# Optimization experiments

Hardware: AMD Instinct MI355X
Metric: run time of the kernel (lower is better)

Reference implementation:

```python
import jax, jax.numpy as jnp
import numpy as np

OUT_F, IN_F = 8192, 4096
TOKENS = 512


def _unpack_int2_to_ternary(packed, alpha, dtype):
    # packed: [out_f, in_f//4] ints 0..255; 4 two-bit codes per byte.
    # code 0 -> -1, code 2 -> +1, codes 1/3 -> 0; then scale by per-row alpha.
    shifts = jnp.arange(4, dtype=packed.dtype) * 2  # [0,2,4,6]
    two_bit = (packed[:, :, None] >> shifts[None, None, :]) & 3  # [out_f, in_f//4, 4]
    two_bit = two_bit.reshape(packed.shape[0], -1)  # [out_f, in_f]
    sign = jnp.where(two_bit == 2, 1.0, jnp.where(two_bit == 0, -1.0, 0.0)).astype(dtype)
    return sign * alpha.astype(dtype)[:, None]


def setup_inputs() -> dict:
    key = jax.random.key(0)
    k1, k2, k3, k4 = jax.random.split(key, 4)
    x = jax.random.normal(k1, (TOKENS, IN_F), dtype=jnp.float32)
    weight_int2 = jax.random.randint(k2, (OUT_F, IN_F // 4), 0, 256, dtype=jnp.int32)
    alpha = jax.random.uniform(k3, (OUT_F,), dtype=jnp.float32, minval=0.01, maxval=0.05)
    bias = jax.random.normal(k4, (OUT_F,), dtype=jnp.float32) * 0.01
    return {"x": x, "weight_int2": weight_int2, "alpha": alpha, "bias": bias}


def reference(x, weight_int2, alpha, bias):
    W = _unpack_int2_to_ternary(weight_int2, alpha, x.dtype)  # [out_f, in_f]
    out = x @ W.T  # [tokens, out_f]
    return out + bias
```

## Files before the change

### kernel.cpp

```cpp
#include <hip/hip_runtime.h>
#include <hip/hip_bf16.h>

typedef unsigned int u32;
typedef unsigned short u16;

#define TOKENS 512
#define OUT_F  8192
#define IN_F   4096
#define KPACK  (IN_F / 4)
#define TMB 128
#define TNB 64
#define BKW 128
#define NWIN (IN_F / BKW)

typedef __attribute__((ext_vector_type(8))) short bf16x8;
typedef __attribute__((ext_vector_type(4))) float f32x4;
typedef __attribute__((ext_vector_type(16))) float f32x16;

__device__ __forceinline__ u32 pack_bf16x2(float a, float b) {
    __hip_bfloat162 h = __float22bfloat162_rn(make_float2(a, b));
    union { __hip_bfloat162 h2; u32 u; } cvt;
    cvt.h2 = h;
    return cvt.u;
}

__device__ __forceinline__ u32 decode_pair(u32 d) {
    u32 s = (__umul24(d, 0x808202u) & 0x06060606u) + 0x01000100u;
    return __builtin_amdgcn_perm(0x00003F80u, 0x0000BF80u, s);
}
__device__ __forceinline__ bf16x8 decode_frag(u32 w, int sh) {
    union { bf16x8 v; u32 u[4]; } c;
    c.u[0] = decode_pair((w >> (sh + 0)) & 0xFu);
    c.u[1] = decode_pair((w >> (sh + 4)) & 0xFu);
    c.u[2] = decode_pair((w >> (sh + 8)) & 0xFu);
    c.u[3] = decode_pair((w >> (sh + 12)) & 0xFu);
    return c.v;
}

__device__ __forceinline__ void async_ld16(const void* g, void* l) {
    __builtin_amdgcn_global_load_lds(
        (const __attribute__((address_space(1))) u32*)g,
        (__attribute__((address_space(3))) u32*)l, 16, 0, 0);
}

__global__ __launch_bounds__(256) void convert_x(const float* __restrict__ X,
                                                 u16* __restrict__ Xb) {
    int i = (blockIdx.x * 256 + threadIdx.x) * 8;
    float4 a = *(const float4*)(X + i);
    float4 b = *(const float4*)(X + i + 4);
    uint4 q;
    q.x = pack_bf16x2(a.x, a.y);
    q.y = pack_bf16x2(a.z, a.w);
    q.z = pack_bf16x2(b.x, b.y);
    q.w = pack_bf16x2(b.z, b.w);
    *(uint4*)(Xb + i) = q;
}

__global__ __launch_bounds__(256) void repack_w9(const u32* __restrict__ W2,
                                                 u32* __restrict__ W9) {
    __shared__ u32 dense[128 * 32];
    const int ngrp = blockIdx.x;
    const int kc   = blockIdx.y;
    const int t = threadIdx.x;
#pragma unroll
    for (int i = 0; i < 16; ++i) {
        int id = t + 256 * i;
        int col = id >> 5, jq = id & 31;
        uint4 wv = *(const uint4*)(W2 + (size_t)(ngrp * 128 + col) * KPACK + kc * 128 + jq * 4);
        dense[col * 32 + (jq ^ (col & 31))] =
            (wv.x & 0xFFu) | ((wv.y & 0xFFu) << 8) | ((wv.z & 0xFFu) << 16) | ((wv.w & 0xFFu) << 24);
    }
    __syncthreads();
    const u16* sp = (const u16*)dense;
#pragma unroll
    for (int p = 0; p < 4; ++p) {
        int e = t + 256 * p;
        int lane = e & 63;
        int kq = (e >> 6) & 3;
        int wp2 = (e >> 8) & 1;
        int nho = (e >> 9) & 1;
        int h = lane >> 5;
        int c0 = nho * 64 + (lane & 31), c1 = c0 + 32;
        int nb = ngrp * 2 + nho;
#pragma unroll
        for (int ws = 0; ws < 2; ++ws) {
            int wloc = wp2 * 2 + ws;
            int w = kc * 4 + wloc;
            int j0 = wloc * 8 + kq * 2;
            u32 x0 = sp[((c0 * 32 + (j0 ^ (c0 & 31))) << 1) | h];
            u32 x1 = sp[((c0 * 32 + ((j0 + 1) ^ (c0 & 31))) << 1) | h];
            u32 y0 = sp[((c1 * 32 + (j0 ^ (c1 & 31))) << 1) | h];
            u32 y1 = sp[((c1 * 32 + ((j0 + 1) ^ (c1 & 31))) << 1) | h];
            W9[((((size_t)nb * 4 + kq) * 2 + 0) * NWIN + w) * 64 + lane] = x0 | (x1 << 16);
            W9[((((size_t)nb * 4 + kq) * 2 + 1) * NWIN + w) * 64 + lane] = y0 | (y1 << 16);
        }
    }
}

__global__ __launch_bounds__(512, 4) void ternary_gemm10(
    const u16* __restrict__ Xb,
    const u32* __restrict__ W9,
    const float* __restrict__ alpha,
    const float* __restrict__ bias,
    float* __restrict__ Out)
{
    __shared__ u16 As[2][TMB * BKW];

    const int tid  = threadIdx.x;
    const int lane = tid & 63;
    const int wave = tid >> 6;
    const int kq = wave & 3;
    const int nh = wave >> 2;

    const int m0 = blockIdx.x * TMB;
    const int nb = blockIdx.y;
    const int n0 = nb * TNB;

    f32x16 acc[4];
#pragma unroll
    for (int mt = 0; mt < 4; ++mt)
#pragma unroll
        for (int i = 0; i < 16; ++i)
            acc[mt][i] = 0.f;

    const u16* gbase = Xb + (size_t)(m0 + wave * 16) * IN_F;
    u32 aoff[4];
    u32 lbase[4];
#pragma unroll
    for (int i = 0; i < 4; ++i) {
        int rr = i * 4 + (lane >> 4);
        int cd = (lane & 15) ^ (rr & 15);
        aoff[i] = rr * IN_F + cd * 8;
        lbase[i] = (wave * 16 + i * 4) * BKW;
    }

    u32 ofsA0[2];
#pragma unroll
    for (int ks = 0; ks < 2; ++ks) {
        int row = lane & 31;
        int chunk = kq * 4 + ks * 2 + (lane >> 5);
        ofsA0[ks] = row * BKW + (chunk ^ (row & 15)) * 8;
    }

    const u32* wq = W9 + ((((size_t)nb * 4 + kq) * 2 + nh) * NWIN) * 64 + lane;

    u32 wcur = wq[0];
    u32 wnext = wq[64];
#pragma unroll
    for (int i = 0; i < 4; ++i) async_ld16(gbase + aoff[i], &As[0][lbase[i]]);
    __syncthreads();

    for (int w = 0; w < NWIN; ++w) {
        const int buf = w & 1;
        if (w + 1 < NWIN) {
            const int koff = (w + 1) * BKW;
#pragma unroll
            for (int i = 0; i < 4; ++i)
                async_ld16(gbase + aoff[i] + koff, &As[buf ^ 1][lbase[i]]);
        }
        u32 wnn = 0;
        if (w + 2 < NWIN) wnn = wq[(size_t)(w + 2) * 64];

        const u16* ab = As[buf];
#pragma unroll
        for (int ks = 0; ks < 2; ++ks) {
            const u16* ap = ab + ofsA0[ks];
            bf16x8 a0 = *(const bf16x8*)(ap);
            bf16x8 a1 = *(const bf16x8*)(ap + 4096);
            bf16x8 a2 = *(const bf16x8*)(ap + 8192);
            bf16x8 a3 = *(const bf16x8*)(ap + 12288);
            bf16x8 b0 = decode_frag(wcur, ks * 16);
            acc[0] = __builtin_amdgcn_mfma_f32_32x32x16_bf16(a0, b0, acc[0], 0, 0, 0);
            acc[1] = __builtin_amdgcn_mfma_f32_32x32x16_bf16(a1, b0, acc[1], 0, 0, 0);
            acc[2] = __builtin_amdgcn_mfma_f32_32x32x16_bf16(a2, b0, acc[2], 0, 0, 0);
            acc[3] = __builtin_amdgcn_mfma_f32_32x32x16_bf16(a3, b0, acc[3], 0, 0, 0);
        }
        wcur = wnext;
        wnext = wnn;
        __syncthreads();
    }

    f32x4* red = (f32x4*)As;
#pragma unroll 1
    for (int q = 1; q < 4; ++q) {
        if (kq == q) {
            f32x4* dst = red + nh * 1024 + lane;
#pragma unroll
            for (int mt = 0; mt < 4; ++mt)
#pragma unroll
                for (int sub = 0; sub < 4; ++sub) {
                    f32x4 v = {acc[mt][sub * 4 + 0], acc[mt][sub * 4 + 1],
                               acc[mt][sub * 4 + 2], acc[mt][sub * 4 + 3]};
                    dst[(mt * 4 + sub) * 64] = v;
                }
        }
        __syncthreads();
        if (kq == 0) {
            const f32x4* src = red + nh * 1024 + lane;
#pragma unroll
            for (int mt = 0; mt < 4; ++mt)
#pragma unroll
                for (int sub = 0; sub < 4; ++sub) {
                    f32x4 v = src[(mt * 4 + sub) * 64];
#pragma unroll
                    for (int i = 0; i < 4; ++i)
                        acc[mt][sub * 4 + i] += v[i];
                }
        }
        __syncthreads();
    }

    if (kq == 0) {
        int ncol = n0 + nh * 32 + (lane & 31);
        float av = alpha[ncol];
        float bv = bias[ncol];
#pragma unroll
        for (int mt = 0; mt < 4; ++mt) {
#pragma unroll
            for (int r = 0; r < 16; ++r) {
                int row = m0 + mt * 32 + (r & 3) + 8 * (r >> 2) + 4 * (lane >> 5);
                Out[(size_t)row * OUT_F + ncol] = acc[mt][r] * av + bv;
            }
        }
    }
}

__global__ void ternary_naive(const float* __restrict__ X, const u32* __restrict__ W2,
                              const float* __restrict__ alpha, const float* __restrict__ bias,
                              float* __restrict__ Out) {
    int o  = blockIdx.x * 64 + (threadIdx.x & 63);
    int tk = blockIdx.y * 4 + (threadIdx.x >> 6);
    const float* x = X + (size_t)tk * IN_F;
    const u32* w = W2 + (size_t)o * KPACK;
    float s = 0.f;
    for (int d = 0; d < KPACK; ++d) {
        u32 b = w[d] & 0xFFu;
        const float* xp = x + d * 4;
#pragma unroll
        for (int j = 0; j < 4; ++j) {
            u32 c = (b >> (2 * j)) & 3u;
            float wv = (c == 2u) ? 1.f : ((c == 0u) ? -1.f : 0.f);
            s += xp[j] * wv;
        }
    }
    Out[(size_t)tk * OUT_F + o] = s * alpha[o] + bias[o];
}

extern "C" void kernel_launch(void* const* d_in, const int* in_sizes, int n_in,
                              void* d_out, int out_size, void* d_ws, size_t ws_size,
                              hipStream_t stream) {
    const float* x = (const float*)d_in[0];
    const u32* w2 = (const u32*)d_in[1];
    const float* alpha = (const float*)d_in[2];
    const float* bias  = (const float*)d_in[3];
    float* out = (float*)d_out;

    const size_t xb_bytes = (size_t)TOKENS * IN_F * sizeof(u16);
    const size_t w9_bytes = (size_t)OUT_F * IN_F / 4;

    if (ws_size >= xb_bytes + w9_bytes) {
        u16* xb = (u16*)d_ws;
        u32* w9 = (u32*)((char*)d_ws + xb_bytes);
        convert_x<<<(TOKENS * IN_F) / (256 * 8), 256, 0, stream>>>(x, xb);
        repack_w9<<<dim3(64, 8), 256, 0, stream>>>(w2, w9);
        ternary_gemm10<<<dim3(TOKENS / TMB, OUT_F / TNB), 512, 0, stream>>>(xb, w9, alpha, bias, out);
    } else {
        ternary_naive<<<dim3(OUT_F / 64, TOKENS / 4), 256, 0, stream>>>(x, w2, alpha, bias, out);
    }
}
```

Measured before the change: 131.3 us.

## Pipeline GEMM loads with explicit vmcnt waits and merge prep kernels

Rewrites the GEMM main loop so each window waits only for the loads it needs (s_waitcnt vmcnt(1) plus raw s_barrier) instead of a full __syncthreads drain. The next A tile's async LDS loads and the B word loads stay in flight across compute. The loop is unrolled by two with a peeled tail, and B words are loaded through inline asm. It also fuses the x-to-bf16 conversion and weight repack into one launch, saving a kernel launch. The risk is fragile hand-managed wait counts and scheduling barriers.

```diff
diff --git a/kernel.cpp b/kernel.cpp
--- a/kernel.cpp
+++ b/kernel.cpp
@@ -43,25 +43,39 @@
         (__attribute__((address_space(3))) u32*)l, 16, 0, 0);
 }
 
-__global__ __launch_bounds__(256) void convert_x(const float* __restrict__ X,
-                                                 u16* __restrict__ Xb) {
-    int i = (blockIdx.x * 256 + threadIdx.x) * 8;
-    float4 a = *(const float4*)(X + i);
-    float4 b = *(const float4*)(X + i + 4);
-    uint4 q;
-    q.x = pack_bf16x2(a.x, a.y);
-    q.y = pack_bf16x2(a.z, a.w);
-    q.z = pack_bf16x2(b.x, b.y);
-    q.w = pack_bf16x2(b.z, b.w);
-    *(uint4*)(Xb + i) = q;
-}
-
-__global__ __launch_bounds__(256) void repack_w9(const u32* __restrict__ W2,
-                                                 u32* __restrict__ W9) {
+__device__ __forceinline__ void async_b(const u32* g, u32& dst) {
+    asm volatile("global_load_dword %0, %1, off"
+                 : "=v"(dst) : "v"(g) : "memory");
+}
+
+#define VMW(N) asm volatile("s_waitcnt vmcnt(" #N ")" ::: "memory")
+
+__global__ __launch_bounds__(256) void prep(const float* __restrict__ X,
+                                            u16* __restrict__ Xb,
+                                            const u32* __restrict__ W2,
+                                            u32* __restrict__ W9) {
     __shared__ u32 dense[128 * 32];
+    const int t = threadIdx.x;
+
+    if (blockIdx.y == 8) {
+        int base = blockIdx.x * 32768 + t * 8;
+#pragma unroll
+        for (int r = 0; r < 16; ++r) {
+            int i = base + r * 2048;
+            float4 a = *(const float4*)(X + i);
+            float4 b = *(const float4*)(X + i + 4);
+            uint4 q;
+            q.x = pack_bf16x2(a.x, a.y);
+            q.y = pack_bf16x2(a.z, a.w);
+            q.z = pack_bf16x2(b.x, b.y);
+            q.w = pack_bf16x2(b.z, b.w);
+            *(uint4*)(Xb + i) = q;
+        }
+        return;
+    }
+
     const int ngrp = blockIdx.x;
     const int kc   = blockIdx.y;
-    const int t = threadIdx.x;
 #pragma unroll
     for (int i = 0; i < 16; ++i) {
         int id = t + 256 * i;
@@ -97,7 +111,7 @@
     }
 }
 
-__global__ __launch_bounds__(512, 4) void ternary_gemm10(
+__global__ __launch_bounds__(512, 4) void ternary_gemm13(
     const u16* __restrict__ Xb,
     const u32* __restrict__ W9,
     const float* __restrict__ alpha,
@@ -144,23 +158,15 @@
 
     const u32* wq = W9 + ((((size_t)nb * 4 + kq) * 2 + nh) * NWIN) * 64 + lane;
 
-    u32 wcur = wq[0];
-    u32 wnext = wq[64];
-#pragma unroll
-    for (int i = 0; i < 4; ++i) async_ld16(gbase + aoff[i], &As[0][lbase[i]]);
-    __syncthreads();
-
-    for (int w = 0; w < NWIN; ++w) {
-        const int buf = w & 1;
-        if (w + 1 < NWIN) {
-            const int koff = (w + 1) * BKW;
-#pragma unroll
-            for (int i = 0; i < 4; ++i)
-                async_ld16(gbase + aoff[i] + koff, &As[buf ^ 1][lbase[i]]);
-        }
-        u32 wnn = 0;
-        if (w + 2 < NWIN) wnn = wq[(size_t)(w + 2) * 64];
-
+    auto issueA = [&](int w) {
+        u16* d = As[w & 1];
+        const int koff = w * BKW;
+#pragma unroll
+        for (int i = 0; i < 4; ++i)
+            async_ld16(gbase + aoff[i] + koff, d + lbase[i]);
+    };
+
+    auto window_compute = [&](int buf, u32 bw) {
         const u16* ab = As[buf];
 #pragma unroll
         for (int ks = 0; ks < 2; ++ks) {
@@ -169,16 +175,45 @@
             bf16x8 a1 = *(const bf16x8*)(ap + 4096);
             bf16x8 a2 = *(const bf16x8*)(ap + 8192);
             bf16x8 a3 = *(const bf16x8*)(ap + 12288);
-            bf16x8 b0 = decode_frag(wcur, ks * 16);
+            bf16x8 b0 = decode_frag(bw, ks * 16);
             acc[0] = __builtin_amdgcn_mfma_f32_32x32x16_bf16(a0, b0, acc[0], 0, 0, 0);
             acc[1] = __builtin_amdgcn_mfma_f32_32x32x16_bf16(a1, b0, acc[1], 0, 0, 0);
             acc[2] = __builtin_amdgcn_mfma_f32_32x32x16_bf16(a2, b0, acc[2], 0, 0, 0);
             acc[3] = __builtin_amdgcn_mfma_f32_32x32x16_bf16(a3, b0, acc[3], 0, 0, 0);
         }
-        wcur = wnext;
-        wnext = wnn;
-        __syncthreads();
-    }
+    };
+
+    u32 bqE, bqO;
+    async_b(wq, bqE);
+    issueA(0);
+    async_b(wq + 64, bqO);
+
+#pragma unroll 1
+    for (int p = 0; p < (NWIN - 2) / 2; ++p) {
+        const int w = 2 * p;
+        VMW(1);
+        __builtin_amdgcn_s_barrier();
+        __builtin_amdgcn_sched_barrier(0);
+        issueA(w + 1);
+        window_compute(0, bqE);
+        async_b(wq + (size_t)(w + 2) * 64, bqE);
+
+        VMW(1);
+        __builtin_amdgcn_s_barrier();
+        __builtin_amdgcn_sched_barrier(0);
+        issueA(w + 2);
+        window_compute(1, bqO);
+        async_b(wq + (size_t)(w + 3) * 64, bqO);
+    }
+    VMW(1);
+    __builtin_amdgcn_s_barrier();
+    __builtin_amdgcn_sched_barrier(0);
+    issueA(31);
+    window_compute(0, bqE);
+    VMW(0);
+    __builtin_amdgcn_s_barrier();
+    __builtin_amdgcn_sched_barrier(0);
+    window_compute(1, bqO);
 
     f32x4* red = (f32x4*)As;
 #pragma unroll 1
@@ -261,9 +296,8 @@
     if (ws_size >= xb_bytes + w9_bytes) {
         u16* xb = (u16*)d_ws;
         u32* w9 = (u32*)((char*)d_ws + xb_bytes);
-        convert_x<<<(TOKENS * IN_F) / (256 * 8), 256, 0, stream>>>(x, xb);
-        repack_w9<<<dim3(64, 8), 256, 0, stream>>>(w2, w9);
-        ternary_gemm10<<<dim3(TOKENS / TMB, OUT_F / TNB), 512, 0, stream>>>(xb, w9, alpha, bias, out);
+        prep<<<dim3(64, 9), 256, 0, stream>>>(x, xb, w2, w9);
+        ternary_gemm13<<<dim3(TOKENS / TMB, OUT_F / TNB), 512, 0, stream>>>(xb, w9, alpha, bias, out);
     } else {
         ternary_naive<<<dim3(OUT_F / 64, TOKENS / 4), 256, 0, stream>>>(x, w2, alpha, bias, out);
     }
```

Result: slower. 134.8 us (+2.7%).
